# Kernel optimization log

Measured on AMD Instinct MI355X. Metric: run time of the kernel, lower is better.

## Reference

```python
import jax, jax.numpy as jnp
import numpy as np

N, E = 100000, 1600000
IN_C, HID, OUT_C = 128, 128, 64
HOPS, L = 2, 3
EPS = 1e-5


def setup_inputs() -> dict:
    key = jax.random.key(0)
    ks = jax.random.split(key, 16)
    x = jax.random.normal(ks[0], (N, IN_C), jnp.float32)
    edge_index = jax.random.randint(ks[1], (2, E), 0, N, dtype=jnp.int32).astype(jnp.int64)
    CAT = HID * (HOPS + 1)  # 384
    def lin(k, fan_in, fan_out, nstack):
        return jax.random.normal(k, (nstack, fan_in, fan_out), jnp.float32) / np.sqrt(fan_in)
    return {
        "x": x,
        "edge_index": edge_index,
        "W0": lin(ks[2], IN_C, HID, HOPS + 1),
        "b0": jnp.zeros((HOPS + 1, HID), jnp.float32),
        "W1": lin(ks[3], CAT, HID, HOPS + 1),
        "b1": jnp.zeros((HOPS + 1, HID), jnp.float32),
        "W2": lin(ks[4], CAT, OUT_C, HOPS + 1),
        "b2": jnp.zeros((HOPS + 1, OUT_C), jnp.float32),
        "bn0_g": jnp.ones((CAT,), jnp.float32),
        "bn0_b": jnp.zeros((CAT,), jnp.float32),
        "bn1_g": jnp.ones((CAT,), jnp.float32),
        "bn1_b": jnp.zeros((CAT,), jnp.float32),
        "fpW": jax.random.normal(ks[5], (OUT_C * (HOPS + 1), OUT_C), jnp.float32) / np.sqrt(OUT_C * (HOPS + 1)),
        "fpb": jnp.zeros((OUT_C,), jnp.float32),
    }


def reference(x, edge_index, W0, b0, W1, b1, W2, b2,
              bn0_g, bn0_b, bn1_g, bn1_b, fpW, fpb):
    row, col = edge_index[0], edge_index[1]
    # gcn_norm with add_self_loops=False, unit edge weights:
    # deg = scatter_add(1, col); w_e = deg^-1/2[row] * deg^-1/2[col]
    deg = jnp.zeros((N,), x.dtype).at[col].add(1.0)
    dinv = jnp.where(deg > 0, jax.lax.rsqrt(jnp.maximum(deg, 1.0)), 0.0)
    ew = dinv[row] * dinv[col]

    def spmm(h):
        # adj_t = SparseTensor(row=col, col=row, value=ew): out[col] += ew * h[row]
        return jax.ops.segment_sum(ew[:, None] * h[row], col, num_segments=N)

    def mixhop(h, W, b):
        outs = []
        for j in range(HOPS + 1):
            hj = h @ W[j] + b[j]          # lins[j](h)
            for _ in range(j):
                hj = spmm(hj)             # A^j applied j times
            outs.append(hj)
        return jnp.concatenate(outs, axis=1)

    def bn(h, g, bb):
        # BatchNorm1d in training mode: batch stats, biased variance
        mu = h.mean(axis=0)
        var = h.var(axis=0)
        return g * (h - mu) * jax.lax.rsqrt(var + EPS) + bb

    h = jax.nn.relu(bn(mixhop(x, W0, b0), bn0_g, bn0_b))   # dropout: identity (eval)
    h = jax.nn.relu(bn(mixhop(h, W1, b1), bn1_g, bn1_b))
    h = mixhop(h, W2, b2)
    return h @ fpW + fpb
```

## Files before the change

kernel.cpp:

```cpp
#include <hip/hip_runtime.h>
#include <cstdint>
#include <cstddef>

#define IN_C 128
#define HIDc 128
#define OUTc 64

using bf8 = __attribute__((ext_vector_type(8))) __bf16;
using f4  = __attribute__((ext_vector_type(4))) float;

__device__ __forceinline__ unsigned short f2bf(float f) {
    unsigned int u = __float_as_uint(f);
    unsigned int r = (u + 0x7FFFu + ((u >> 16) & 1u)) >> 16;
    return (unsigned short)r;
}
__device__ __forceinline__ float bf2f(unsigned short h) {
    return __uint_as_float(((unsigned int)h) << 16);
}

__device__ __forceinline__ void gload16(const unsigned short* g, unsigned short* l) {
    __builtin_amdgcn_global_load_lds(
        (const __attribute__((address_space(1))) unsigned int*)g,
        (__attribute__((address_space(3))) unsigned int*)l, 16, 0, 0);
}

__global__ void k_detect(const long long* ei, int n_nodes, int* flag) {
    int t = threadIdx.x;
    long long v = ei[t];
    int ok = (v >= 0 && v < (long long)n_nodes) ? 1 : 0;
    unsigned long long m = __ballot(ok);
    if (t == 0) *flag = (m == ~0ull) ? 1 : 0;
}

__global__ void k_cvt_hist(const void* ei, int twoE, int E, const int* flag,
                           int* __restrict__ out, int* __restrict__ deg, int n) {
    int i = blockIdx.x * blockDim.x + threadIdx.x;
    if (i >= twoE) return;
    int v = (*flag) ? (int)((const long long*)ei)[i] : ((const int*)ei)[i];
    out[i] = v;
    if (i >= E && (unsigned)v < (unsigned)n) atomicAdd(&deg[v], 1);
}

__global__ void k_dinv(const int* __restrict__ deg, float* __restrict__ dinv, int n) {
    int i = blockIdx.x * blockDim.x + threadIdx.x;
    if (i < n) dinv[i] = (deg[i] > 0) ? rsqrtf((float)deg[i]) : 0.0f;
}

__global__ void k_alloc(const int* __restrict__ deg, int* __restrict__ base,
                        int* __restrict__ cursor, int* __restrict__ counter, int n) {
    int i = blockIdx.x * blockDim.x + threadIdx.x;
    int lane = threadIdx.x & 63;
    int val = (i < n) ? deg[i] : 0;
    int scan = val;
    #pragma unroll
    for (int off = 1; off < 64; off <<= 1) {
        int t = __shfl_up(scan, off);
        if (lane >= off) scan += t;
    }
    int excl = scan - val;
    int total = __shfl(scan, 63);
    int wb = 0;
    if (lane == 0) wb = atomicAdd(counter, total);
    wb = __shfl(wb, 0);
    if (i < n) { base[i] = wb + excl; cursor[i] = wb + excl; }
}

__global__ void k_scatter(const int* __restrict__ eint, int E,
                          const float* __restrict__ dinv, int n,
                          int* __restrict__ cursor, int2* __restrict__ ew) {
    int e = blockIdx.x * blockDim.x + threadIdx.x;
    if (e >= E) return;
    int r = eint[e];
    int c = eint[E + e];
    if ((unsigned)r >= (unsigned)n || (unsigned)c >= (unsigned)n) return;
    int p = atomicAdd(&cursor[c], 1);
    int2 v; v.x = r; v.y = __float_as_int(dinv[r] * dinv[c]);
    ew[p] = v;
}

__global__ void k_wprep(const float* __restrict__ W, unsigned short* __restrict__ Wt,
                        int K, int N) {
    int j = blockIdx.y;
    int idx = blockIdx.x * 256 + threadIdx.x;
    if (idx >= K * N) return;
    int k = idx / N, nn = idx - k * N;
    Wt[(size_t)j * N * K + (size_t)nn * K + k] = f2bf(W[(size_t)j * K * N + idx]);
}

__global__ void k_cast4(const float* __restrict__ x, unsigned short* __restrict__ y, int n4) {
    int i = blockIdx.x * 256 + threadIdx.x;
    if (i >= n4) return;
    float4 v = ((const float4*)x)[i];
    ushort4 o;
    o.x = f2bf(v.x); o.y = f2bf(v.y); o.z = f2bf(v.z); o.w = f2bf(v.w);
    ((ushort4*)y)[i] = o;
}

template<int TILEN, bool BFOUT>
__global__ __launch_bounds__(256) void k_gemm(
    const unsigned short* __restrict__ A0, const unsigned short* __restrict__ A1,
    const unsigned short* __restrict__ A2, int W, int M, int K,
    const unsigned short* __restrict__ Bt,
    const float* __restrict__ bias,
    unsigned short* __restrict__ C0, int ldc0,
    unsigned short* __restrict__ C1, int ldc1,
    unsigned short* __restrict__ C2, int ldc2,
    float* __restrict__ Cf, int ldcf)
{
    constexpr int TM = 4;
    constexpr int TN = TILEN / 32;
    __shared__ __align__(16) unsigned short As[128 * 32];
    __shared__ __align__(16) unsigned short Bs[TILEN * 32];
    __shared__ __align__(16) unsigned char  Cs[16384];

    int bx, j;
    if (gridDim.y == 3) {
        int L = blockIdx.x + gridDim.x * blockIdx.y;
        int c = L & 7, s = L >> 3;
        j  = s % 3;
        bx = c + 8 * (s / 3);
        if (bx * 128 >= M) return;
    } else {
        bx = blockIdx.x; j = blockIdx.y;
    }

    int t = threadIdx.x;
    int wave = t >> 6, lane = t & 63;
    int m16 = lane & 15, q = lane >> 4;
    int row0 = bx * 128;
    int wr = (wave & 1) * 64;
    int wc = (wave >> 1) * (TILEN / 2);

    int lr = lane >> 2, lch = lane & 3;
    int ra0 = (wave * 2 + 0) * 16 + lr;
    int ra1 = (wave * 2 + 1) * 16 + lr;
    int ga0 = row0 + ra0; if (ga0 >= M) ga0 = M - 1;
    int ga1 = row0 + ra1; if (ga1 >= M) ga1 = M - 1;
    size_t boff0 = (size_t)(j * TILEN + ra0) * K;
    size_t boff1 = (size_t)(j * TILEN + ra1) * K;
    size_t boffS = (size_t)(j * TILEN + wave * 16 + lr) * K;

    f4 acc[TM][TN];
    #pragma unroll
    for (int i = 0; i < TM; i++)
        #pragma unroll
        for (int jj = 0; jj < TN; jj++) acc[i][jj] = (f4){0.f, 0.f, 0.f, 0.f};

    for (int kk = 0; kk < K; kk += 32) {
        int pi = kk / W;
        const unsigned short* Ap = (pi == 0) ? A0 : ((pi == 1) ? A1 : A2);
        int kl = kk - pi * W;

        __syncthreads();
        gload16(&Ap[(size_t)ga0 * W + kl + lch * 8], &As[(wave * 2 + 0) * 512]);
        gload16(&Ap[(size_t)ga1 * W + kl + lch * 8], &As[(wave * 2 + 1) * 512]);
        if (TILEN == 128) {
            gload16(&Bt[boff0 + kk + lch * 8], &Bs[(wave * 2 + 0) * 512]);
            gload16(&Bt[boff1 + kk + lch * 8], &Bs[(wave * 2 + 1) * 512]);
        } else {
            gload16(&Bt[boffS + kk + lch * 8], &Bs[wave * 512]);
        }
        __syncthreads();

        bf8 af[TM], bfr[TN];
        #pragma unroll
        for (int tm = 0; tm < TM; tm++)
            af[tm] = *(const bf8*)&As[(wr + tm * 16 + m16) * 32 + q * 8];
        #pragma unroll
        for (int tn = 0; tn < TN; tn++)
            bfr[tn] = *(const bf8*)&Bs[(wc + tn * 16 + m16) * 32 + q * 8];
        #pragma unroll
        for (int tm = 0; tm < TM; tm++)
            #pragma unroll
            for (int tn = 0; tn < TN; tn++)
                acc[tm][tn] = __builtin_amdgcn_mfma_f32_16x16x32_bf16(
                    af[tm], bfr[tn], acc[tm][tn], 0, 0, 0);
    }

    constexpr int EB  = BFOUT ? 2 : 4;
    constexpr int RB  = TILEN * EB;
    constexpr int CPR = RB / 16;
    constexpr int PT  = 64 * CPR / 256;
    char* Cb;
    long  ldb;
    if (BFOUT) {
        unsigned short* Cj = (j == 0) ? C0 : ((j == 1) ? C1 : C2);
        int lj = (j == 0) ? ldc0 : ((j == 1) ? ldc1 : ldc2);
        Cb = (char*)Cj; ldb = (long)lj * 2;
    } else {
        Cb = (char*)Cf; ldb = (long)ldcf * 4;
    }
    #pragma unroll
    for (int half = 0; half < 2; half++) {
        __syncthreads();
        if ((wave & 1) == half) {
            #pragma unroll
            for (int tn = 0; tn < TN; tn++) {
                int col = wc + tn * 16 + m16;
                float bi = bias[j * TILEN + col];
                #pragma unroll
                for (int tm = 0; tm < TM; tm++) {
                    #pragma unroll
                    for (int r = 0; r < 4; r++) {
                        int lrow = tm * 16 + q * 4 + r;
                        float v = acc[tm][tn][r] + bi;
                        if (BFOUT) ((unsigned short*)Cs)[lrow * TILEN + col] = f2bf(v);
                        else       ((float*)Cs)[lrow * TILEN + col] = v;
                    }
                }
            }
        }
        __syncthreads();
        #pragma unroll
        for (int i = 0; i < PT; i++) {
            int idx  = i * 256 + t;
            int lrow = idx / CPR;
            int c16  = idx - lrow * CPR;
            int grow = row0 + half * 64 + lrow;
            if (grow < M)
                *(uint4*)(Cb + (size_t)grow * ldb + c16 * 16) = ((const uint4*)Cs)[idx];
        }
    }
}

template<int PW>
__global__ __launch_bounds__(256) void k_spmm2v(
    const unsigned short* __restrict__ S,
    unsigned short* __restrict__ D1, unsigned short* __restrict__ D2,
    const int* __restrict__ base, const int* __restrict__ deg,
    const int2* __restrict__ ew, int n)
{
    constexpr int ROWB = 2 * PW;
    constexpr int GS   = ROWB / 8;
    constexpr int EP   = 64 / GS;
    constexpr int UN   = 16 / EP;

    int node = blockIdx.x * 4 + threadIdx.y;
    if (node >= n) return;
    int lane = threadIdx.x;
    int sub  = lane / GS;
    int li   = lane % GS;
    const unsigned short* Sp = S + li * 8;

    float acc[8];
    #pragma unroll
    for (int v = 0; v < 8; v++) acc[v] = 0.f;

    int b = base[node], d = deg[node];
    if (d > 0) {
        int end = b + d;
        for (int e = b; e < end; e += UN * EP) {
            int row[UN]; float wt[UN];
            #pragma unroll
            for (int u = 0; u < UN; u++) {
                int myE = e + u * EP + sub;
                int cl  = myE < end ? myE : end - 1;
                int2 ev = ew[cl];
                row[u] = ev.x;
                wt[u]  = (myE < end) ? __int_as_float(ev.y) : 0.f;
            }
            uint4 g[UN];
            #pragma unroll
            for (int u = 0; u < UN; u++)
                g[u] = *(const uint4*)(Sp + (size_t)row[u] * ROWB);
            #pragma unroll
            for (int u = 0; u < UN; u++) {
                float we = wt[u];
                const unsigned int* gw = (const unsigned int*)&g[u];
                #pragma unroll
                for (int p = 0; p < 4; p++) {
                    acc[2 * p]     += we * bf2f((unsigned short)(gw[p] & 0xffff));
                    acc[2 * p + 1] += we * bf2f((unsigned short)(gw[p] >> 16));
                }
            }
        }
    }
    #pragma unroll
    for (int m = GS; m < 64; m <<= 1)
        #pragma unroll
        for (int v = 0; v < 8; v++) acc[v] += __shfl_xor(acc[v], m);

    if (lane < GS) {
        int cu = li * 8;
        unsigned short* D = (cu < PW) ? (D1 + (size_t)node * PW + cu)
                                      : (D2 + (size_t)node * PW + (cu - PW));
        uint4 o;
        o.x = (unsigned)f2bf(acc[0]) | ((unsigned)f2bf(acc[1]) << 16);
        o.y = (unsigned)f2bf(acc[2]) | ((unsigned)f2bf(acc[3]) << 16);
        o.z = (unsigned)f2bf(acc[4]) | ((unsigned)f2bf(acc[5]) << 16);
        o.w = (unsigned)f2bf(acc[6]) | ((unsigned)f2bf(acc[7]) << 16);
        *(uint4*)D = o;
    }
}

template<int W>
__global__ __launch_bounds__(256) void k_spmmv(
    const unsigned short* __restrict__ S, unsigned short* __restrict__ D,
    const int* __restrict__ base, const int* __restrict__ deg,
    const int2* __restrict__ ew, int n)
{
    constexpr int GS = W / 8;
    constexpr int EP = 64 / GS;
    constexpr int UN = (EP == 4) ? 4 : 2;

    int node = blockIdx.x * 4 + threadIdx.y;
    if (node >= n) return;
    int lane = threadIdx.x;
    int sub  = lane / GS;
    int li   = lane % GS;
    const unsigned short* Sp = S + li * 8;

    float acc[8];
    #pragma unroll
    for (int v = 0; v < 8; v++) acc[v] = 0.f;

    int b = base[node], d = deg[node];
    if (d > 0) {
        int end = b + d;
        for (int e = b; e < end; e += UN * EP) {
            int row[UN]; float wt[UN];
            #pragma unroll
            for (int u = 0; u < UN; u++) {
                int myE = e + u * EP + sub;
                int cl  = myE < end ? myE : end - 1;
                int2 ev = ew[cl];
                row[u] = ev.x;
                wt[u]  = (myE < end) ? __int_as_float(ev.y) : 0.f;
            }
            uint4 g[UN];
            #pragma unroll
            for (int u = 0; u < UN; u++)
                g[u] = *(const uint4*)(Sp + (size_t)row[u] * W);
            #pragma unroll
            for (int u = 0; u < UN; u++) {
                float we = wt[u];
                const unsigned int* gw = (const unsigned int*)&g[u];
                #pragma unroll
                for (int p = 0; p < 4; p++) {
                    acc[2 * p]     += we * bf2f((unsigned short)(gw[p] & 0xffff));
                    acc[2 * p + 1] += we * bf2f((unsigned short)(gw[p] >> 16));
                }
            }
        }
    }
    #pragma unroll
    for (int m = GS; m < 64; m <<= 1)
        #pragma unroll
        for (int v = 0; v < 8; v++) acc[v] += __shfl_xor(acc[v], m);

    if (lane < GS) {
        uint4 o;
        o.x = (unsigned)f2bf(acc[0]) | ((unsigned)f2bf(acc[1]) << 16);
        o.y = (unsigned)f2bf(acc[2]) | ((unsigned)f2bf(acc[3]) << 16);
        o.z = (unsigned)f2bf(acc[4]) | ((unsigned)f2bf(acc[5]) << 16);
        o.w = (unsigned)f2bf(acc[6]) | ((unsigned)f2bf(acc[7]) << 16);
        *(uint4*)(D + (size_t)node * W + li * 8) = o;
    }
}

__global__ void k_bnstats_v(const unsigned short* __restrict__ p0,
                            const unsigned short* __restrict__ p1,
                            const unsigned short* __restrict__ p2,
                            float* __restrict__ sums, float* __restrict__ sumsq, int n)
{
    __shared__ float ls[384], ls2[384];
    int t = threadIdx.x;
    ls[t] = 0.f; ls2[t] = 0.f;
    __syncthreads();
    int o = t % 48, g = t / 48;
    int pi = o >> 4, io = o & 15;
    const unsigned short* src = (pi == 0) ? p0 : ((pi == 1) ? p1 : p2);
    float s[8], s2[8];
    #pragma unroll
    for (int j = 0; j < 8; j++) { s[j] = 0.f; s2[j] = 0.f; }
    for (int r = blockIdx.x * 8 + g; r < n; r += gridDim.x * 8) {
        uint4 v = *(const uint4*)(src + (size_t)r * 128 + io * 8);
        const unsigned int* w = (const unsigned int*)&v;
        #pragma unroll
        for (int p = 0; p < 4; p++) {
            float a = bf2f((unsigned short)(w[p] & 0xffff));
            float b = bf2f((unsigned short)(w[p] >> 16));
            s[2 * p] += a;     s2[2 * p] += a * a;
            s[2 * p + 1] += b; s2[2 * p + 1] += b * b;
        }
    }
    #pragma unroll
    for (int j = 0; j < 8; j++) {
        atomicAdd(&ls[o * 8 + j], s[j]);
        atomicAdd(&ls2[o * 8 + j], s2[j]);
    }
    __syncthreads();
    atomicAdd(&sums[t], ls[t]);
    atomicAdd(&sumsq[t], ls2[t]);
}

__global__ void k_bnfin(const float* __restrict__ sums, const float* __restrict__ sumsq,
                        const float* __restrict__ g, const float* __restrict__ bb,
                        float* __restrict__ scale, float* __restrict__ shift,
                        int cat, float invn)
{
    int c = threadIdx.x;
    if (c >= cat) return;
    float mu  = sums[c] * invn;
    float var = sumsq[c] * invn - mu * mu;
    float sc  = g[c] * rsqrtf(var + 1e-5f);
    scale[c] = sc;
    shift[c] = bb[c] - mu * sc;
}

__global__ void k_bnapply_v(unsigned short* __restrict__ p0,
                            unsigned short* __restrict__ p1,
                            unsigned short* __restrict__ p2,
                            const float* __restrict__ scale,
                            const float* __restrict__ shift, int n)
{
    int t = threadIdx.x;
    int o = t % 48, g = t / 48;
    int pi = o >> 4, io = o & 15;
    unsigned short* src = (pi == 0) ? p0 : ((pi == 1) ? p1 : p2);
    float sc[8], sh[8];
    #pragma unroll
    for (int j = 0; j < 8; j++) { sc[j] = scale[o * 8 + j]; sh[j] = shift[o * 8 + j]; }
    for (int r = blockIdx.x * 8 + g; r < n; r += gridDim.x * 8) {
        uint4 v = *(const uint4*)(src + (size_t)r * 128 + io * 8);
        unsigned int* w = (unsigned int*)&v;
        uint4 ov; unsigned int* ow = (unsigned int*)&ov;
        #pragma unroll
        for (int p = 0; p < 4; p++) {
            float a = fmaxf(bf2f((unsigned short)(w[p] & 0xffff)) * sc[2 * p] + sh[2 * p], 0.f);
            float b = fmaxf(bf2f((unsigned short)(w[p] >> 16)) * sc[2 * p + 1] + sh[2 * p + 1], 0.f);
            ow[p] = (unsigned)f2bf(a) | ((unsigned)f2bf(b) << 16);
        }
        *(uint4*)(src + (size_t)r * 128 + io * 8) = ov;
    }
}

__global__ void k_diag(float* out, float val, int n) {
    int i = blockIdx.x * blockDim.x + threadIdx.x;
    if (i < n) out[i] = val;
}

extern "C" void kernel_launch(void* const* d_in, const int* in_sizes, int n_in,
                              void* d_out, int out_size, void* d_ws, size_t ws_size,
                              hipStream_t stream)
{
    const float* x    = (const float*)d_in[0];
    const void*  ei   = d_in[1];
    const float* W0   = (const float*)d_in[2];
    const float* b0   = (const float*)d_in[3];
    const float* W1   = (const float*)d_in[4];
    const float* b1   = (const float*)d_in[5];
    const float* W2   = (const float*)d_in[6];
    const float* b2   = (const float*)d_in[7];
    const float* bn0g = (const float*)d_in[8];
    const float* bn0b = (const float*)d_in[9];
    const float* bn1g = (const float*)d_in[10];
    const float* bn1b = (const float*)d_in[11];
    const float* fpW  = (const float*)d_in[12];
    const float* fpb  = (const float*)d_in[13];
    float* out = (float*)d_out;

    const int N    = in_sizes[0] / IN_C;
    const int twoE = in_sizes[1];
    const int E    = twoE / 2;

    char* p = (char*)d_ws;
    auto alloc = [&](size_t bytes) -> char* {
        char* r = p; p += (bytes + 255) & ~(size_t)255; return r;
    };
    unsigned short* u0 = (unsigned short*)alloc((size_t)6 * N * 128 * 2);
    unsigned short* u1 = u0 + (size_t)1 * N * 128;
    unsigned short* u2 = u0 + (size_t)2 * N * 128;
    unsigned short* u3 = u0 + (size_t)3 * N * 128;
    unsigned short* u4 = u0 + (size_t)4 * N * 128;
    unsigned short* u5 = u0 + (size_t)5 * N * 128;
    unsigned short* Wt0 = (unsigned short*)alloc((size_t)3 * 128 * 128 * 2);
    unsigned short* Wt1 = (unsigned short*)alloc((size_t)3 * 384 * 128 * 2);
    unsigned short* Wt2 = (unsigned short*)alloc((size_t)3 * 384 * 64 * 2);
    unsigned short* WtF = (unsigned short*)alloc((size_t)192 * 64 * 2);
    float* dinv  = (float*)alloc((size_t)N * 4);
    int2*  ew    = (int2*)alloc((size_t)E * 8);
    float* sums  = (float*)alloc(2 * 384 * 4);
    float* sumsq = sums + 384;
    float* scale = (float*)alloc(384 * 4);
    float* shift = (float*)alloc(384 * 4);
    int* deg     = (int*)alloc((size_t)N * 4);
    int* base    = (int*)alloc((size_t)N * 4);
    int* cursor  = (int*)alloc((size_t)N * 4);
    int* eint    = (int*)alloc((size_t)twoE * 4);
    int* counter = (int*)alloc(4);
    int* flag    = (int*)alloc(4);

    size_t required = (size_t)(p - (char*)d_ws);
    if (required > ws_size) {
        k_diag<<<(out_size + 255) / 256, 256, 0, stream>>>(
            out, (float)(ws_size >> 20), out_size);
        return;
    }

    const int T = 256;
    dim3 spmm_blk(64, 4);
    int  spmm_grid = (N + 3) / 4;
    int  gx  = (N + 127) / 128;
    int  gx8 = ((gx + 7) / 8) * 8;

    k_wprep<<<dim3((128 * 128 + 255) / 256, 3), T, 0, stream>>>(W0, Wt0, 128, 128);
    k_wprep<<<dim3((384 * 128 + 255) / 256, 3), T, 0, stream>>>(W1, Wt1, 384, 128);
    k_wprep<<<dim3((384 * 64  + 255) / 256, 3), T, 0, stream>>>(W2, Wt2, 384, 64);
    k_wprep<<<dim3((192 * 64  + 255) / 256, 1), T, 0, stream>>>(fpW, WtF, 192, 64);
    unsigned short* Xb = u3;
    k_cast4<<<((N * 128 / 4) + 255) / 256, T, 0, stream>>>(x, Xb, N * 128 / 4);

    hipMemsetAsync(deg, 0, (size_t)N * 4, stream);
    hipMemsetAsync(counter, 0, 4, stream);
    k_detect<<<1, 64, 0, stream>>>((const long long*)ei, N, flag);
    k_cvt_hist<<<(twoE + T - 1) / T, T, 0, stream>>>(ei, twoE, E, flag, eint, deg, N);
    k_dinv<<<(N + T - 1) / T, T, 0, stream>>>(deg, dinv, N);
    k_alloc<<<(N + T - 1) / T, T, 0, stream>>>(deg, base, cursor, counter, N);
    k_scatter<<<(E + T - 1) / T, T, 0, stream>>>(eint, E, dinv, N, cursor, ew);

    k_gemm<128, true><<<dim3(gx8, 3), T, 0, stream>>>(Xb, Xb, Xb, 128, N, 128,
        Wt0, b0, u0, 128, u1, 256, u1 + 128, 256, nullptr, 0);
    k_spmm2v<128><<<spmm_grid, spmm_blk, 0, stream>>>(u1, u4, u5, base, deg, ew, N);
    k_spmmv<128><<<spmm_grid, spmm_blk, 0, stream>>>(u5, u3, base, deg, ew, N);
    hipMemsetAsync(sums, 0, 2 * 384 * 4, stream);
    k_bnstats_v<<<2048, 384, 0, stream>>>(u0, u4, u3, sums, sumsq, N);
    k_bnfin<<<1, 384, 0, stream>>>(sums, sumsq, bn0g, bn0b, scale, shift, 384, 1.0f / N);
    k_bnapply_v<<<2048, 384, 0, stream>>>(u0, u4, u3, scale, shift, N);

    k_gemm<128, true><<<dim3(gx8, 3), T, 0, stream>>>(u0, u4, u3, 128, N, 384,
        Wt1, b1, u5, 128, u1, 256, u1 + 128, 256, nullptr, 0);
    k_spmm2v<128><<<spmm_grid, spmm_blk, 0, stream>>>(u1, u0, u4, base, deg, ew, N);
    k_spmmv<128><<<spmm_grid, spmm_blk, 0, stream>>>(u4, u3, base, deg, ew, N);
    hipMemsetAsync(sums, 0, 2 * 384 * 4, stream);
    k_bnstats_v<<<2048, 384, 0, stream>>>(u5, u0, u3, sums, sumsq, N);
    k_bnfin<<<1, 384, 0, stream>>>(sums, sumsq, bn1g, bn1b, scale, shift, 384, 1.0f / N);
    k_bnapply_v<<<2048, 384, 0, stream>>>(u5, u0, u3, scale, shift, N);

    k_gemm<64, true><<<dim3(gx8, 3), T, 0, stream>>>(u5, u0, u3, 128, N, 384,
        Wt2, b2, u1, 64, u2, 128, u2 + 64, 128, nullptr, 0);
    k_spmm2v<64><<<spmm_grid, spmm_blk, 0, stream>>>(u2, u4, u4 + (size_t)N * 64,
                                                     base, deg, ew, N);
    k_spmmv<64><<<spmm_grid, spmm_blk, 0, stream>>>(u4 + (size_t)N * 64, u5,
                                                    base, deg, ew, N);

    k_gemm<64, false><<<dim3(gx, 1), T, 0, stream>>>(u1, u4, u5, 64, N, 192,
        WtF, fpb, nullptr, 0, nullptr, 0, nullptr, 0, out, 64);
}
```

Measured before the change: 1.136 ms.

## Compute all three hop projections per block with 64-row tiles

The GEMM kernel now handles all three weight slices (NP) in a single block over a 64-row tile. Each A tile is loaded once and reused across the three outputs, where before a separate block per hop reloaded the same A rows. The old 2D grid with swizzled block ordering is replaced by a 1D grid of 64-row blocks. In exchange each block keeps more accumulators and uses more B shared memory, which raises register pressure and may lower occupancy.

Result: no change. 1.154 ms (+1.6%).

```diff
diff --git a/kernel.cpp b/kernel.cpp
--- a/kernel.cpp
+++ b/kernel.cpp
@@ -96,8 +96,8 @@
     ((ushort4*)y)[i] = o;
 }
 
-template<int TILEN, bool BFOUT>
-__global__ __launch_bounds__(256) void k_gemm(
+template<int TILEN, int NP, bool BFOUT>
+__global__ __launch_bounds__(256) void k_gemm3(
     const unsigned short* __restrict__ A0, const unsigned short* __restrict__ A1,
     const unsigned short* __restrict__ A2, int W, int M, int K,
     const unsigned short* __restrict__ Bt,
@@ -108,43 +108,32 @@
     float* __restrict__ Cf, int ldcf)
 {
     constexpr int TM = 4;
-    constexpr int TN = TILEN / 32;
-    __shared__ __align__(16) unsigned short As[128 * 32];
-    __shared__ __align__(16) unsigned short Bs[TILEN * 32];
+    constexpr int TN = TILEN / 64;
+    constexpr int NB = NP * TILEN / 64;
+    __shared__ __align__(16) unsigned short As[64 * 32];
+    __shared__ __align__(16) unsigned short Bs[NP * TILEN * 32];
     __shared__ __align__(16) unsigned char  Cs[16384];
-
-    int bx, j;
-    if (gridDim.y == 3) {
-        int L = blockIdx.x + gridDim.x * blockIdx.y;
-        int c = L & 7, s = L >> 3;
-        j  = s % 3;
-        bx = c + 8 * (s / 3);
-        if (bx * 128 >= M) return;
-    } else {
-        bx = blockIdx.x; j = blockIdx.y;
-    }
 
     int t = threadIdx.x;
     int wave = t >> 6, lane = t & 63;
     int m16 = lane & 15, q = lane >> 4;
-    int row0 = bx * 128;
-    int wr = (wave & 1) * 64;
-    int wc = (wave >> 1) * (TILEN / 2);
+    int row0 = blockIdx.x * 64;
+    int wc = wave * (TILEN / 4);
 
     int lr = lane >> 2, lch = lane & 3;
-    int ra0 = (wave * 2 + 0) * 16 + lr;
-    int ra1 = (wave * 2 + 1) * 16 + lr;
-    int ga0 = row0 + ra0; if (ga0 >= M) ga0 = M - 1;
-    int ga1 = row0 + ra1; if (ga1 >= M) ga1 = M - 1;
-    size_t boff0 = (size_t)(j * TILEN + ra0) * K;
-    size_t boff1 = (size_t)(j * TILEN + ra1) * K;
-    size_t boffS = (size_t)(j * TILEN + wave * 16 + lr) * K;
-
-    f4 acc[TM][TN];
-    #pragma unroll
-    for (int i = 0; i < TM; i++)
-        #pragma unroll
-        for (int jj = 0; jj < TN; jj++) acc[i][jj] = (f4){0.f, 0.f, 0.f, 0.f};
+    int ga = row0 + wave * 16 + lr; if (ga >= M) ga = M - 1;
+    size_t boffB[NB];
+    #pragma unroll
+    for (int i = 0; i < NB; i++)
+        boffB[i] = (size_t)((wave * NB + i) * 16 + lr) * K;
+
+    f4 acc[NP][TM][TN];
+    #pragma unroll
+    for (int j = 0; j < NP; j++)
+        #pragma unroll
+        for (int i = 0; i < TM; i++)
+            #pragma unroll
+            for (int jj = 0; jj < TN; jj++) acc[j][i][jj] = (f4){0.f, 0.f, 0.f, 0.f};
 
     for (int kk = 0; kk < K; kk += 32) {
         int pi = kk / W;
@@ -152,61 +141,59 @@
         int kl = kk - pi * W;
 
         __syncthreads();
-        gload16(&Ap[(size_t)ga0 * W + kl + lch * 8], &As[(wave * 2 + 0) * 512]);
-        gload16(&Ap[(size_t)ga1 * W + kl + lch * 8], &As[(wave * 2 + 1) * 512]);
-        if (TILEN == 128) {
-            gload16(&Bt[boff0 + kk + lch * 8], &Bs[(wave * 2 + 0) * 512]);
-            gload16(&Bt[boff1 + kk + lch * 8], &Bs[(wave * 2 + 1) * 512]);
-        } else {
-            gload16(&Bt[boffS + kk + lch * 8], &Bs[wave * 512]);
-        }
+        gload16(&Ap[(size_t)ga * W + kl + lch * 8], &As[wave * 512]);
+        #pragma unroll
+        for (int i = 0; i < NB; i++)
+            gload16(&Bt[boffB[i] + kk + lch * 8], &Bs[(wave * NB + i) * 512]);
         __syncthreads();
 
-        bf8 af[TM], bfr[TN];
+        bf8 af[TM], bfr[NP][TN];
         #pragma unroll
         for (int tm = 0; tm < TM; tm++)
-            af[tm] = *(const bf8*)&As[(wr + tm * 16 + m16) * 32 + q * 8];
-        #pragma unroll
-        for (int tn = 0; tn < TN; tn++)
-            bfr[tn] = *(const bf8*)&Bs[(wc + tn * 16 + m16) * 32 + q * 8];
-        #pragma unroll
-        for (int tm = 0; tm < TM; tm++)
+            af[tm] = *(const bf8*)&As[(tm * 16 + m16) * 32 + q * 8];
+        #pragma unroll
+        for (int j = 0; j < NP; j++)
             #pragma unroll
             for (int tn = 0; tn < TN; tn++)
-                acc[tm][tn] = __builtin_amdgcn_mfma_f32_16x16x32_bf16(
-                    af[tm], bfr[tn], acc[tm][tn], 0, 0, 0);
+                bfr[j][tn] = *(const bf8*)&Bs[(j * TILEN + wc + tn * 16 + m16) * 32 + q * 8];
+        #pragma unroll
+        for (int j = 0; j < NP; j++)
+            #pragma unroll
+            for (int tm = 0; tm < TM; tm++)
+                #pragma unroll
+                for (int tn = 0; tn < TN; tn++)
+                    acc[j][tm][tn] = __builtin_amdgcn_mfma_f32_16x16x32_bf16(
+                        af[tm], bfr[j][tn], acc[j][tm][tn], 0, 0, 0);
     }
 
     constexpr int EB  = BFOUT ? 2 : 4;
     constexpr int RB  = TILEN * EB;
     constexpr int CPR = RB / 16;
     constexpr int PT  = 64 * CPR / 256;
-    char* Cb;
-    long  ldb;
-    if (BFOUT) {
-        unsigned short* Cj = (j == 0) ? C0 : ((j == 1) ? C1 : C2);
-        int lj = (j == 0) ? ldc0 : ((j == 1) ? ldc1 : ldc2);
-        Cb = (char*)Cj; ldb = (long)lj * 2;
-    } else {
-        Cb = (char*)Cf; ldb = (long)ldcf * 4;
-    }
-    #pragma unroll
-    for (int half = 0; half < 2; half++) {
+    #pragma unroll
+    for (int j = 0; j < NP; j++) {
+        char* Cb;
+        long  ldb;
+        if (BFOUT) {
+            unsigned short* Cj = (j == 0) ? C0 : ((j == 1) ? C1 : C2);
+            int lj = (j == 0) ? ldc0 : ((j == 1) ? ldc1 : ldc2);
+            Cb = (char*)Cj; ldb = (long)lj * 2;
+        } else {
+            Cb = (char*)Cf; ldb = (long)ldcf * 4;
+        }
         __syncthreads();
-        if ((wave & 1) == half) {
-            #pragma unroll
-            for (int tn = 0; tn < TN; tn++) {
-                int col = wc + tn * 16 + m16;
-                float bi = bias[j * TILEN + col];
+        #pragma unroll
+        for (int tn = 0; tn < TN; tn++) {
+            int col = wc + tn * 16 + m16;
+            float bi = bias[j * TILEN + col];
+            #pragma unroll
+            for (int tm = 0; tm < TM; tm++) {
                 #pragma unroll
-                for (int tm = 0; tm < TM; tm++) {
-                    #pragma unroll
-                    for (int r = 0; r < 4; r++) {
-                        int lrow = tm * 16 + q * 4 + r;
-                        float v = acc[tm][tn][r] + bi;
-                        if (BFOUT) ((unsigned short*)Cs)[lrow * TILEN + col] = f2bf(v);
-                        else       ((float*)Cs)[lrow * TILEN + col] = v;
-                    }
+                for (int r = 0; r < 4; r++) {
+                    int lrow = tm * 16 + q * 4 + r;
+                    float v = acc[j][tm][tn][r] + bi;
+                    if (BFOUT) ((unsigned short*)Cs)[lrow * TILEN + col] = f2bf(v);
+                    else       ((float*)Cs)[lrow * TILEN + col] = v;
                 }
             }
         }
@@ -216,7 +203,7 @@
             int idx  = i * 256 + t;
             int lrow = idx / CPR;
             int c16  = idx - lrow * CPR;
-            int grow = row0 + half * 64 + lrow;
+            int grow = row0 + lrow;
             if (grow < M)
                 *(uint4*)(Cb + (size_t)grow * ldb + c16 * 16) = ((const uint4*)Cs)[idx];
         }
@@ -501,8 +488,7 @@
     const int T = 256;
     dim3 spmm_blk(64, 4);
     int  spmm_grid = (N + 3) / 4;
-    int  gx  = (N + 127) / 128;
-    int  gx8 = ((gx + 7) / 8) * 8;
+    int  g64 = (N + 63) / 64;
 
     k_wprep<<<dim3((128 * 128 + 255) / 256, 3), T, 0, stream>>>(W0, Wt0, 128, 128);
     k_wprep<<<dim3((384 * 128 + 255) / 256, 3), T, 0, stream>>>(W1, Wt1, 384, 128);
@@ -519,7 +505,7 @@
     k_alloc<<<(N + T - 1) / T, T, 0, stream>>>(deg, base, cursor, counter, N);
     k_scatter<<<(E + T - 1) / T, T, 0, stream>>>(eint, E, dinv, N, cursor, ew);
 
-    k_gemm<128, true><<<dim3(gx8, 3), T, 0, stream>>>(Xb, Xb, Xb, 128, N, 128,
+    k_gemm3<128, 3, true><<<g64, T, 0, stream>>>(Xb, Xb, Xb, 128, N, 128,
         Wt0, b0, u0, 128, u1, 256, u1 + 128, 256, nullptr, 0);
     k_spmm2v<128><<<spmm_grid, spmm_blk, 0, stream>>>(u1, u4, u5, base, deg, ew, N);
     k_spmmv<128><<<spmm_grid, spmm_blk, 0, stream>>>(u5, u3, base, deg, ew, N);
@@ -528,7 +514,7 @@
     k_bnfin<<<1, 384, 0, stream>>>(sums, sumsq, bn0g, bn0b, scale, shift, 384, 1.0f / N);
     k_bnapply_v<<<2048, 384, 0, stream>>>(u0, u4, u3, scale, shift, N);
 
-    k_gemm<128, true><<<dim3(gx8, 3), T, 0, stream>>>(u0, u4, u3, 128, N, 384,
+    k_gemm3<128, 3, true><<<g64, T, 0, stream>>>(u0, u4, u3, 128, N, 384,
         Wt1, b1, u5, 128, u1, 256, u1 + 128, 256, nullptr, 0);
     k_spmm2v<128><<<spmm_grid, spmm_blk, 0, stream>>>(u1, u0, u4, base, deg, ew, N);
     k_spmmv<128><<<spmm_grid, spmm_blk, 0, stream>>>(u4, u3, base, deg, ew, N);
@@ -537,13 +523,13 @@
     k_bnfin<<<1, 384, 0, stream>>>(sums, sumsq, bn1g, bn1b, scale, shift, 384, 1.0f / N);
     k_bnapply_v<<<2048, 384, 0, stream>>>(u5, u0, u3, scale, shift, N);
 
-    k_gemm<64, true><<<dim3(gx8, 3), T, 0, stream>>>(u5, u0, u3, 128, N, 384,
+    k_gemm3<64, 3, true><<<g64, T, 0, stream>>>(u5, u0, u3, 128, N, 384,
         Wt2, b2, u1, 64, u2, 128, u2 + 64, 128, nullptr, 0);
     k_spmm2v<64><<<spmm_grid, spmm_blk, 0, stream>>>(u2, u4, u4 + (size_t)N * 64,
                                                      base, deg, ew, N);
     k_spmmv<64><<<spmm_grid, spmm_blk, 0, stream>>>(u4 + (size_t)N * 64, u5,
                                                     base, deg, ew, N);
 
-    k_gemm<64, false><<<dim3(gx, 1), T, 0, stream>>>(u1, u4, u5, 64, N, 192,
+    k_gemm3<64, 1, false><<<g64, T, 0, stream>>>(u1, u4, u5, 64, N, 192,
         WtF, fpb, nullptr, 0, nullptr, 0, nullptr, 0, out, 64);
 }
```
